# Kernel tuning notes

Hardware: AMD Instinct MI355X
Metric: run time of the kernel (lower is better)

Reference implementation:

```python
import jax, jax.numpy as jnp
import numpy as np

B, N, F, D = 8, 2048, 128, 128


def setup_inputs() -> dict:
    key = jax.random.key(0)
    k1, k2, k3 = jax.random.split(key, 3)
    inputs = jax.random.normal(k1, (B, N, F), dtype=jnp.float32)
    adj = jax.random.uniform(k2, (B, N, N), dtype=jnp.float32)  # nonneg weights -> positive degrees
    W_kernel = jax.random.normal(k3, (F, D), dtype=jnp.float32) * (1.0 / np.sqrt(F))
    W_bias = jnp.zeros((D,), dtype=jnp.float32)
    return {"inputs": inputs, "adj": adj, "W_kernel": W_kernel, "W_bias": W_bias}


def _normalize_adjacency(adj):
    # D^{-1/2} A D^{-1/2}: same math as diag-matmul chain, via broadcast scaling
    d = jnp.sum(adj, axis=-1)                      # [B, N]
    d_sqrt_inv = jnp.power(d, -0.5)
    d_sqrt_inv = jnp.where(jnp.isinf(d_sqrt_inv), 0.0, d_sqrt_inv)
    return d_sqrt_inv[..., :, None] * adj * d_sqrt_inv[..., None, :]


def reference(inputs, adj, W_kernel, W_bias):
    adj_norm = _normalize_adjacency(adj)           # [B, N, N]
    feats = inputs @ W_kernel + W_bias             # [B, N, D]
    out = jnp.einsum('bnm,bmd->bnd', adj_norm, feats)
    return jax.nn.relu(out)
```

## Files before the change

kernel.cpp:

```cpp
#include <hip/hip_runtime.h>
#include <hip/hip_bf16.h>
#include <stdint.h>

#define B_ 8
#define N_ 2048
#define F_ 128
#define D_ 128

typedef short bf16x8 __attribute__((ext_vector_type(8)));
typedef float f32x4 __attribute__((ext_vector_type(4)));

__device__ __forceinline__ unsigned short f2bf(float f) {
    unsigned u = __float_as_uint(f);
    u += 0x7fffu + ((u >> 16) & 1u);
    return (unsigned short)(u >> 16);
}

__global__ __launch_bounds__(256) void k_deg(const float* __restrict__ adj,
                                             float* __restrict__ rs) {
    const int wave = threadIdx.x >> 6, lane = threadIdx.x & 63;
    const int row = blockIdx.x * 4 + wave;
    const float4* p = (const float4*)(adj + (size_t)row * N_);
    float s = 0.f;
#pragma unroll
    for (int j = 0; j < 8; ++j) {
        float4 v = p[j * 64 + lane];
        s += (v.x + v.y) + (v.z + v.w);
    }
#pragma unroll
    for (int m = 1; m < 64; m <<= 1) s += __shfl_xor(s, m, 64);
    if (lane == 0) rs[row] = (s > 0.f) ? (1.0f / sqrtf(s)) : 0.f;
}

__global__ __launch_bounds__(256) void k_feat(const float* __restrict__ x,
                                              const float* __restrict__ W,
                                              const float* __restrict__ bias,
                                              const float* __restrict__ rs,
                                              unsigned short* __restrict__ gt) {
    __shared__ __align__(16) unsigned char sX[64 * 128 * 2];
    __shared__ __align__(16) unsigned char sW[128 * 128 * 2];
    const int t = threadIdx.x;
    const int R0 = blockIdx.x * 64;

#pragma unroll
    for (int j = 0; j < 4; ++j) {
        int c = j * 256 + t;
        int row = c >> 4, sub = c & 15;
        const float4* src = (const float4*)(x + (size_t)(R0 + row) * F_ + sub * 8);
        float4 v0 = src[0], v1 = src[1];
        union { bf16x8 v; unsigned short u[8]; } pk;
        pk.u[0] = f2bf(v0.x); pk.u[1] = f2bf(v0.y); pk.u[2] = f2bf(v0.z); pk.u[3] = f2bf(v0.w);
        pk.u[4] = f2bf(v1.x); pk.u[5] = f2bf(v1.y); pk.u[6] = f2bf(v1.z); pk.u[7] = f2bf(v1.w);
        unsigned byte = (unsigned)(row * 256 + sub * 16);
        byte ^= ((byte >> 8) & 7u) << 4;
        *(bf16x8*)(sX + byte) = pk.v;
    }
#pragma unroll
    for (int j = 0; j < 8; ++j) {
        int c = j * 256 + t;
        int d = c >> 4, sub = c & 15;
        union { bf16x8 v; unsigned short u[8]; } pk;
#pragma unroll
        for (int e = 0; e < 8; ++e) pk.u[e] = f2bf(W[(size_t)(sub * 8 + e) * D_ + d]);
        unsigned byte = (unsigned)(d * 256 + sub * 16);
        byte ^= ((byte >> 8) & 7u) << 4;
        *(bf16x8*)(sW + byte) = pk.v;
    }
    __syncthreads();

    const int w = t >> 6, l = t & 63, lr = l & 15, lh = l >> 4;
    f32x4 acc[8];
#pragma unroll
    for (int j = 0; j < 8; ++j) acc[j] = (f32x4){0.f, 0.f, 0.f, 0.f};

#pragma unroll
    for (int ks = 0; ks < 4; ++ks) {
        int f0 = lh * 8 + ks * 32;
        unsigned abyte = (unsigned)((w * 16 + lr) * 256 + f0 * 2);
        abyte ^= ((abyte >> 8) & 7u) << 4;
        bf16x8 a = *(const bf16x8*)(sX + abyte);
#pragma unroll
        for (int j = 0; j < 8; ++j) {
            unsigned bbyte = (unsigned)((j * 16 + lr) * 256 + f0 * 2);
            bbyte ^= ((bbyte >> 8) & 7u) << 4;
            bf16x8 bb = *(const bf16x8*)(sW + bbyte);
            acc[j] = __builtin_amdgcn_mfma_f32_16x16x32_bf16(a, bb, acc[j], 0, 0, 0);
        }
    }

#pragma unroll
    for (int j = 0; j < 8; ++j) {
        int d = j * 16 + lr;
        float bv = bias[d];
#pragma unroll
        for (int r = 0; r < 4; ++r) {
            int m = R0 + w * 16 + lh * 4 + r;
            float v = (acc[j][r] + bv) * rs[m];
            int b = m >> 11, n = m & (N_ - 1);
            gt[((size_t)b * D_ + d) * N_ + n] = f2bf(v);
        }
    }
}

__global__ __launch_bounds__(256) void k_gcn(const float* __restrict__ adj,
                                             const unsigned short* __restrict__ gt,
                                             const float* __restrict__ rs,
                                             float* __restrict__ out) {
    __shared__ __align__(16) unsigned char sA[2][32 * 64 * 2];
    __shared__ __align__(16) unsigned char sB[2][128 * 64 * 2];

    unsigned bid = blockIdx.x;
    unsigned wg = (bid & 7u) * 64u + (bid >> 3);
    const int b = (int)(wg >> 6);
    const int nt = (int)(wg & 63u);
    const int R0 = nt * 32;

    const float* adjB = adj + (size_t)b * N_ * N_ + (size_t)R0 * N_;
    const unsigned short* gtB = gt + (size_t)b * D_ * N_;

    const int t = threadIdx.x;
    const int w = t >> 6, l = t & 63, lr = l & 15, lh = l >> 4;

    auto stage = [&](int bufidx, int k0) {
        unsigned char* sBb = sB[bufidx];
#pragma unroll
        for (int i = 0; i < 4; ++i) {
            int c = i * 256 + t;
            int d = c >> 3, sub = c & 7;
            int sub2 = sub ^ (d & 7);
            const unsigned short* g = gtB + (size_t)d * N_ + k0 + sub2 * 8;
            __builtin_amdgcn_global_load_lds(
                (const __attribute__((address_space(1))) void*)g,
                (__attribute__((address_space(3))) void*)(sBb + c * 16), 16, 0, 0);
        }
        {
            int c = t;
            int row = c >> 3, sub = c & 7;
            const float4* src = (const float4*)(adjB + (size_t)row * N_ + k0 + sub * 8);
            float4 v0 = src[0], v1 = src[1];
            union { bf16x8 v; unsigned short u[8]; } pk;
            pk.u[0] = f2bf(v0.x); pk.u[1] = f2bf(v0.y); pk.u[2] = f2bf(v0.z); pk.u[3] = f2bf(v0.w);
            pk.u[4] = f2bf(v1.x); pk.u[5] = f2bf(v1.y); pk.u[6] = f2bf(v1.z); pk.u[7] = f2bf(v1.w);
            unsigned byte = (unsigned)(row * 128 + sub * 16);
            byte ^= ((byte >> 7) & 7u) << 4;
            *(bf16x8*)(sA[bufidx] + byte) = pk.v;
        }
    };

    f32x4 acc[2][2];
#pragma unroll
    for (int i = 0; i < 2; ++i)
#pragma unroll
        for (int jn = 0; jn < 2; ++jn) acc[i][jn] = (f32x4){0.f, 0.f, 0.f, 0.f};

    stage(0, 0);
    __syncthreads();

    const int NITER = N_ / 64;
    for (int it = 0; it < NITER; ++it) {
        int cur = it & 1;
        if (it + 1 < NITER) stage(cur ^ 1, (it + 1) * 64);

        const unsigned char* pA = sA[cur];
        const unsigned char* pB = sB[cur];
#pragma unroll
        for (int kk = 0; kk < 2; ++kk) {
            bf16x8 a[2], bb[2];
#pragma unroll
            for (int i = 0; i < 2; ++i) {
                unsigned byte = (unsigned)((i * 16 + lr) * 128 + lh * 16 + kk * 64);
                byte ^= ((byte >> 7) & 7u) << 4;
                a[i] = *(const bf16x8*)(pA + byte);
            }
#pragma unroll
            for (int jn = 0; jn < 2; ++jn) {
                int d = w * 32 + jn * 16 + lr;
                unsigned byte = (unsigned)(d * 128 + lh * 16 + kk * 64);
                byte ^= ((byte >> 7) & 7u) << 4;
                bb[jn] = *(const bf16x8*)(pB + byte);
            }
#pragma unroll
            for (int i = 0; i < 2; ++i)
#pragma unroll
                for (int jn = 0; jn < 2; ++jn)
                    acc[i][jn] = __builtin_amdgcn_mfma_f32_16x16x32_bf16(a[i], bb[jn], acc[i][jn], 0, 0, 0);
        }
        __syncthreads();
    }

#pragma unroll
    for (int i = 0; i < 2; ++i) {
#pragma unroll
        for (int r = 0; r < 4; ++r) {
            int row = i * 16 + lh * 4 + r;
            float rsn = rs[b * N_ + R0 + row];
#pragma unroll
            for (int jn = 0; jn < 2; ++jn) {
                int d = w * 32 + jn * 16 + lr;
                float v = acc[i][jn][r] * rsn;
                out[((size_t)(b * N_ + R0 + row)) * D_ + d] = fmaxf(v, 0.f);
            }
        }
    }
}

extern "C" void kernel_launch(void* const* d_in, const int* in_sizes, int n_in,
                              void* d_out, int out_size, void* d_ws, size_t ws_size,
                              hipStream_t stream) {
    const float* inputs = (const float*)d_in[0];
    const float* adj    = (const float*)d_in[1];
    const float* Wk     = (const float*)d_in[2];
    const float* Wb     = (const float*)d_in[3];
    float* out = (float*)d_out;

    float* rs = (float*)d_ws;
    unsigned short* gt = (unsigned short*)((char*)d_ws + 65536);

    k_deg <<<(B_ * N_) / 4, 256, 0, stream>>>(adj, rs);
    k_feat<<<(B_ * N_) / 64, 256, 0, stream>>>(inputs, Wk, Wb, rs, gt);
    k_gcn <<<B_ * (N_ / 32), 256, 0, stream>>>(adj, gt, rs, out);
}
```

Measured before the change: 67.18 us.

## Pre-transpose W to bf16, move column scaling into adj staging, widen GCN tiles

The degree kernel now also converts W to a transposed bf16 copy once, and k_feat loads it into LDS with direct global-to-LDS loads instead of each block redoing the strided transpose and conversion. The right-side D^{-1/2} scaling moves from the feature GEMM epilogue into the adjacency staging of the GCN kernel, where rs values are multiplied into adj before bf16 conversion. The GCN kernel goes to 512 threads with a 128-wide K step, so each wave owns a 16x32 output tile and there are half as many barriers. This doubles LDS per block and adds a per-element multiply plus extra rs loads in the adj path, which may lower occupancy.

```diff
diff --git a/kernel.cpp b/kernel.cpp
--- a/kernel.cpp
+++ b/kernel.cpp
@@ -16,32 +16,52 @@
     return (unsigned short)(u >> 16);
 }
 
-__global__ __launch_bounds__(256) void k_deg(const float* __restrict__ adj,
-                                             float* __restrict__ rs) {
-    const int wave = threadIdx.x >> 6, lane = threadIdx.x & 63;
-    const int row = blockIdx.x * 4 + wave;
-    const float4* p = (const float4*)(adj + (size_t)row * N_);
-    float s = 0.f;
-#pragma unroll
-    for (int j = 0; j < 8; ++j) {
-        float4 v = p[j * 64 + lane];
-        s += (v.x + v.y) + (v.z + v.w);
-    }
-#pragma unroll
-    for (int m = 1; m < 64; m <<= 1) s += __shfl_xor(s, m, 64);
-    if (lane == 0) rs[row] = (s > 0.f) ? (1.0f / sqrtf(s)) : 0.f;
+__global__ __launch_bounds__(256) void k_degwt(const float* __restrict__ adj,
+                                               const float* __restrict__ W,
+                                               float* __restrict__ rs,
+                                               unsigned short* __restrict__ Wt) {
+    if (blockIdx.x < 4096) {
+        const int wave = threadIdx.x >> 6, lane = threadIdx.x & 63;
+        const int row = blockIdx.x * 4 + wave;
+        const float4* p = (const float4*)(adj + (size_t)row * N_);
+        float s = 0.f;
+#pragma unroll
+        for (int j = 0; j < 8; ++j) {
+            float4 v = p[j * 64 + lane];
+            s += (v.x + v.y) + (v.z + v.w);
+        }
+#pragma unroll
+        for (int m = 1; m < 64; m <<= 1) s += __shfl_xor(s, m, 64);
+        if (lane == 0) rs[row] = (s > 0.f) ? (1.0f / sqrtf(s)) : 0.f;
+    } else {
+        int c = (blockIdx.x - 4096) * 256 + threadIdx.x;
+        int d = c >> 4, f0 = (c & 15) * 8;
+        union { bf16x8 v; unsigned short u[8]; } pk;
+#pragma unroll
+        for (int e = 0; e < 8; ++e) pk.u[e] = f2bf(W[(size_t)(f0 + e) * D_ + d]);
+        *(bf16x8*)(Wt + (size_t)d * F_ + f0) = pk.v;
+    }
 }
 
 __global__ __launch_bounds__(256) void k_feat(const float* __restrict__ x,
-                                              const float* __restrict__ W,
+                                              const unsigned short* __restrict__ Wt,
                                               const float* __restrict__ bias,
-                                              const float* __restrict__ rs,
                                               unsigned short* __restrict__ gt) {
     __shared__ __align__(16) unsigned char sX[64 * 128 * 2];
     __shared__ __align__(16) unsigned char sW[128 * 128 * 2];
     const int t = threadIdx.x;
     const int R0 = blockIdx.x * 64;
 
+#pragma unroll
+    for (int j = 0; j < 8; ++j) {
+        int c = j * 256 + t;
+        unsigned L = (unsigned)c * 16u;
+        unsigned lg = L ^ (((L >> 8) & 7u) << 4);
+        const unsigned char* src = (const unsigned char*)Wt + lg;
+        __builtin_amdgcn_global_load_lds(
+            (const __attribute__((address_space(1))) void*)src,
+            (__attribute__((address_space(3))) void*)(sW + L), 16, 0, 0);
+    }
 #pragma unroll
     for (int j = 0; j < 4; ++j) {
         int c = j * 256 + t;
@@ -55,17 +75,6 @@
         byte ^= ((byte >> 8) & 7u) << 4;
         *(bf16x8*)(sX + byte) = pk.v;
     }
-#pragma unroll
-    for (int j = 0; j < 8; ++j) {
-        int c = j * 256 + t;
-        int d = c >> 4, sub = c & 15;
-        union { bf16x8 v; unsigned short u[8]; } pk;
-#pragma unroll
-        for (int e = 0; e < 8; ++e) pk.u[e] = f2bf(W[(size_t)(sub * 8 + e) * D_ + d]);
-        unsigned byte = (unsigned)(d * 256 + sub * 16);
-        byte ^= ((byte >> 8) & 7u) << 4;
-        *(bf16x8*)(sW + byte) = pk.v;
-    }
     __syncthreads();
 
     const int w = t >> 6, l = t & 63, lr = l & 15, lh = l >> 4;
@@ -95,19 +104,19 @@
 #pragma unroll
         for (int r = 0; r < 4; ++r) {
             int m = R0 + w * 16 + lh * 4 + r;
-            float v = (acc[j][r] + bv) * rs[m];
+            float v = acc[j][r] + bv;
             int b = m >> 11, n = m & (N_ - 1);
             gt[((size_t)b * D_ + d) * N_ + n] = f2bf(v);
         }
     }
 }
 
-__global__ __launch_bounds__(256) void k_gcn(const float* __restrict__ adj,
+__global__ __launch_bounds__(512) void k_gcn(const float* __restrict__ adj,
                                              const unsigned short* __restrict__ gt,
                                              const float* __restrict__ rs,
                                              float* __restrict__ out) {
-    __shared__ __align__(16) unsigned char sA[2][32 * 64 * 2];
-    __shared__ __align__(16) unsigned char sB[2][128 * 64 * 2];
+    __shared__ __align__(16) unsigned char sA[2][32 * 128 * 2];
+    __shared__ __align__(16) unsigned char sB[2][128 * 128 * 2];
 
     unsigned bid = blockIdx.x;
     unsigned wg = (bid & 7u) * 64u + (bid >> 3);
@@ -117,89 +126,83 @@
 
     const float* adjB = adj + (size_t)b * N_ * N_ + (size_t)R0 * N_;
     const unsigned short* gtB = gt + (size_t)b * D_ * N_;
+    const float* rsB = rs + b * N_;
 
     const int t = threadIdx.x;
     const int w = t >> 6, l = t & 63, lr = l & 15, lh = l >> 4;
+    const int wr = (w >> 2) * 16, wc = (w & 3) * 32;
 
     auto stage = [&](int bufidx, int k0) {
         unsigned char* sBb = sB[bufidx];
 #pragma unroll
         for (int i = 0; i < 4; ++i) {
-            int c = i * 256 + t;
-            int d = c >> 3, sub = c & 7;
-            int sub2 = sub ^ (d & 7);
-            const unsigned short* g = gtB + (size_t)d * N_ + k0 + sub2 * 8;
+            int c = i * 512 + t;
+            unsigned L = (unsigned)c * 16u;
+            unsigned lg = L ^ (((L >> 8) & 7u) << 4);
+            int d = (int)(lg >> 8);
+            int mloc = (int)(lg & 255u) >> 1;
+            const unsigned short* g = gtB + (size_t)d * N_ + k0 + mloc;
             __builtin_amdgcn_global_load_lds(
                 (const __attribute__((address_space(1))) void*)g,
-                (__attribute__((address_space(3))) void*)(sBb + c * 16), 16, 0, 0);
+                (__attribute__((address_space(3))) void*)(sBb + L), 16, 0, 0);
         }
         {
-            int c = t;
-            int row = c >> 3, sub = c & 7;
+            int row = t >> 4, sub = t & 15;
             const float4* src = (const float4*)(adjB + (size_t)row * N_ + k0 + sub * 8);
+            const float4* rsm = (const float4*)(rsB + k0 + sub * 8);
             float4 v0 = src[0], v1 = src[1];
+            float4 r0 = rsm[0], r1 = rsm[1];
             union { bf16x8 v; unsigned short u[8]; } pk;
-            pk.u[0] = f2bf(v0.x); pk.u[1] = f2bf(v0.y); pk.u[2] = f2bf(v0.z); pk.u[3] = f2bf(v0.w);
-            pk.u[4] = f2bf(v1.x); pk.u[5] = f2bf(v1.y); pk.u[6] = f2bf(v1.z); pk.u[7] = f2bf(v1.w);
-            unsigned byte = (unsigned)(row * 128 + sub * 16);
-            byte ^= ((byte >> 7) & 7u) << 4;
+            pk.u[0] = f2bf(v0.x * r0.x); pk.u[1] = f2bf(v0.y * r0.y);
+            pk.u[2] = f2bf(v0.z * r0.z); pk.u[3] = f2bf(v0.w * r0.w);
+            pk.u[4] = f2bf(v1.x * r1.x); pk.u[5] = f2bf(v1.y * r1.y);
+            pk.u[6] = f2bf(v1.z * r1.z); pk.u[7] = f2bf(v1.w * r1.w);
+            unsigned byte = (unsigned)(row * 256 + sub * 16);
+            byte ^= ((byte >> 8) & 7u) << 4;
             *(bf16x8*)(sA[bufidx] + byte) = pk.v;
         }
     };
 
-    f32x4 acc[2][2];
-#pragma unroll
-    for (int i = 0; i < 2; ++i)
-#pragma unroll
-        for (int jn = 0; jn < 2; ++jn) acc[i][jn] = (f32x4){0.f, 0.f, 0.f, 0.f};
+    f32x4 acc[2];
+    acc[0] = (f32x4){0.f, 0.f, 0.f, 0.f};
+    acc[1] = (f32x4){0.f, 0.f, 0.f, 0.f};
 
     stage(0, 0);
     __syncthreads();
 
-    const int NITER = N_ / 64;
+    const int NITER = N_ / 128;
     for (int it = 0; it < NITER; ++it) {
         int cur = it & 1;
-        if (it + 1 < NITER) stage(cur ^ 1, (it + 1) * 64);
+        if (it + 1 < NITER) stage(cur ^ 1, (it + 1) * 128);
 
         const unsigned char* pA = sA[cur];
         const unsigned char* pB = sB[cur];
 #pragma unroll
-        for (int kk = 0; kk < 2; ++kk) {
-            bf16x8 a[2], bb[2];
-#pragma unroll
-            for (int i = 0; i < 2; ++i) {
-                unsigned byte = (unsigned)((i * 16 + lr) * 128 + lh * 16 + kk * 64);
-                byte ^= ((byte >> 7) & 7u) << 4;
-                a[i] = *(const bf16x8*)(pA + byte);
+        for (int kk = 0; kk < 4; ++kk) {
+            unsigned abyte = (unsigned)((wr + lr) * 256 + lh * 16 + kk * 64);
+            abyte ^= ((abyte >> 8) & 7u) << 4;
+            bf16x8 a = *(const bf16x8*)(pA + abyte);
+#pragma unroll
+            for (int jn = 0; jn < 2; ++jn) {
+                int d = wc + jn * 16 + lr;
+                unsigned bbyte = (unsigned)(d * 256 + lh * 16 + kk * 64);
+                bbyte ^= ((bbyte >> 8) & 7u) << 4;
+                bf16x8 bb = *(const bf16x8*)(pB + bbyte);
+                acc[jn] = __builtin_amdgcn_mfma_f32_16x16x32_bf16(a, bb, acc[jn], 0, 0, 0);
             }
-#pragma unroll
-            for (int jn = 0; jn < 2; ++jn) {
-                int d = w * 32 + jn * 16 + lr;
-                unsigned byte = (unsigned)(d * 128 + lh * 16 + kk * 64);
-                byte ^= ((byte >> 7) & 7u) << 4;
-                bb[jn] = *(const bf16x8*)(pB + byte);
-            }
-#pragma unroll
-            for (int i = 0; i < 2; ++i)
-#pragma unroll
-                for (int jn = 0; jn < 2; ++jn)
-                    acc[i][jn] = __builtin_amdgcn_mfma_f32_16x16x32_bf16(a[i], bb[jn], acc[i][jn], 0, 0, 0);
         }
         __syncthreads();
     }
 
 #pragma unroll
-    for (int i = 0; i < 2; ++i) {
-#pragma unroll
-        for (int r = 0; r < 4; ++r) {
-            int row = i * 16 + lh * 4 + r;
-            float rsn = rs[b * N_ + R0 + row];
-#pragma unroll
-            for (int jn = 0; jn < 2; ++jn) {
-                int d = w * 32 + jn * 16 + lr;
-                float v = acc[i][jn][r] * rsn;
-                out[((size_t)(b * N_ + R0 + row)) * D_ + d] = fmaxf(v, 0.f);
-            }
+    for (int r = 0; r < 4; ++r) {
+        int row = wr + lh * 4 + r;
+        float rsn = rsB[R0 + row];
+#pragma unroll
+        for (int jn = 0; jn < 2; ++jn) {
+            int d = wc + jn * 16 + lr;
+            float v = acc[jn][r] * rsn;
+            out[((size_t)(b * N_ + R0 + row)) * D_ + d] = fmaxf(v, 0.f);
         }
     }
 }
@@ -215,8 +218,9 @@
 
     float* rs = (float*)d_ws;
     unsigned short* gt = (unsigned short*)((char*)d_ws + 65536);
-
-    k_deg <<<(B_ * N_) / 4, 256, 0, stream>>>(adj, rs);
-    k_feat<<<(B_ * N_) / 64, 256, 0, stream>>>(inputs, Wk, Wb, rs, gt);
-    k_gcn <<<B_ * (N_ / 32), 256, 0, stream>>>(adj, gt, rs, out);
-}
+    unsigned short* Wt = (unsigned short*)((char*)d_ws + 65536 + (size_t)B_ * D_ * N_ * 2);
+
+    k_degwt<<<4096 + 8, 256, 0, stream>>>(adj, Wk, rs, Wt);
+    k_feat <<<(B_ * N_) / 64, 256, 0, stream>>>(inputs, Wt, Wb, gt);
+    k_gcn  <<<B_ * (N_ / 32), 512, 0, stream>>>(adj, gt, rs, out);
+}
```

New measurement: 56.73 us. 1.18x faster.

## Merge degree and feature kernels, restructure GCN matmul with async LDS staging

Applied to the files above, without the earlier changes.

The degree and feature-projection kernels are merged into one launch, and the column D^{-1/2} scaling moves out of the feature kernel into the GCN kernel, which now applies it to fp32 adjacency tiles read from LDS. The GCN kernel switches to 64-row tiles with 512 threads, K-steps of 128, and direct global-to-LDS async loads of fp32 adjacency, with explicit waitcnt/barrier double buffering. The W load is also made coalesced. This aims to cut launch overhead and register-path conversion stalls, at the cost of a large LDS footprint (one block per CU) and only 256 blocks in the main kernel.

```diff
diff --git a/kernel.cpp b/kernel.cpp
--- a/kernel.cpp
+++ b/kernel.cpp
@@ -16,32 +16,48 @@
     return (unsigned short)(u >> 16);
 }
 
-__global__ __launch_bounds__(256) void k_deg(const float* __restrict__ adj,
-                                             float* __restrict__ rs) {
-    const int wave = threadIdx.x >> 6, lane = threadIdx.x & 63;
-    const int row = blockIdx.x * 4 + wave;
-    const float4* p = (const float4*)(adj + (size_t)row * N_);
-    float s = 0.f;
-#pragma unroll
-    for (int j = 0; j < 8; ++j) {
-        float4 v = p[j * 64 + lane];
-        s += (v.x + v.y) + (v.z + v.w);
-    }
-#pragma unroll
-    for (int m = 1; m < 64; m <<= 1) s += __shfl_xor(s, m, 64);
-    if (lane == 0) rs[row] = (s > 0.f) ? (1.0f / sqrtf(s)) : 0.f;
-}
-
-__global__ __launch_bounds__(256) void k_feat(const float* __restrict__ x,
-                                              const float* __restrict__ W,
-                                              const float* __restrict__ bias,
-                                              const float* __restrict__ rs,
-                                              unsigned short* __restrict__ gt) {
+__global__ __launch_bounds__(256) void k_degfeat(const float* __restrict__ adj,
+                                                 const float* __restrict__ x,
+                                                 const float* __restrict__ W,
+                                                 const float* __restrict__ bias,
+                                                 float* __restrict__ rs,
+                                                 unsigned short* __restrict__ gt) {
     __shared__ __align__(16) unsigned char sX[64 * 128 * 2];
     __shared__ __align__(16) unsigned char sW[128 * 128 * 2];
+
     const int t = threadIdx.x;
-    const int R0 = blockIdx.x * 64;
-
+    if (blockIdx.x < 4096) {
+        const int wave = t >> 6, lane = t & 63;
+        const int row = blockIdx.x * 4 + wave;
+        const float4* p = (const float4*)(adj + (size_t)row * N_);
+        float s = 0.f;
+#pragma unroll
+        for (int j = 0; j < 8; ++j) {
+            float4 v = p[j * 64 + lane];
+            s += (v.x + v.y) + (v.z + v.w);
+        }
+#pragma unroll
+        for (int m = 1; m < 64; m <<= 1) s += __shfl_xor(s, m, 64);
+        if (lane == 0) rs[row] = (s > 0.f) ? (1.0f / sqrtf(s)) : 0.f;
+        return;
+    }
+
+    const int R0 = (blockIdx.x - 4096) * 64;
+
+#pragma unroll
+    for (int i = 0; i < 16; ++i) {
+        int c = i * 256 + t;
+        int f = c >> 5, d0 = (c & 31) * 4;
+        float4 v = *(const float4*)(W + (size_t)f * D_ + d0);
+        float vv[4] = {v.x, v.y, v.z, v.w};
+#pragma unroll
+        for (int e = 0; e < 4; ++e) {
+            int dd = d0 + e;
+            unsigned byte = (unsigned)(dd * 256 + f * 2);
+            byte ^= ((byte >> 8) & 15u) << 4;
+            *(unsigned short*)(sW + byte) = f2bf(vv[e]);
+        }
+    }
 #pragma unroll
     for (int j = 0; j < 4; ++j) {
         int c = j * 256 + t;
@@ -55,17 +71,6 @@
         byte ^= ((byte >> 8) & 7u) << 4;
         *(bf16x8*)(sX + byte) = pk.v;
     }
-#pragma unroll
-    for (int j = 0; j < 8; ++j) {
-        int c = j * 256 + t;
-        int d = c >> 4, sub = c & 15;
-        union { bf16x8 v; unsigned short u[8]; } pk;
-#pragma unroll
-        for (int e = 0; e < 8; ++e) pk.u[e] = f2bf(W[(size_t)(sub * 8 + e) * D_ + d]);
-        unsigned byte = (unsigned)(d * 256 + sub * 16);
-        byte ^= ((byte >> 8) & 7u) << 4;
-        *(bf16x8*)(sW + byte) = pk.v;
-    }
     __syncthreads();
 
     const int w = t >> 6, l = t & 63, lr = l & 15, lh = l >> 4;
@@ -75,14 +80,13 @@
 
 #pragma unroll
     for (int ks = 0; ks < 4; ++ks) {
-        int f0 = lh * 8 + ks * 32;
-        unsigned abyte = (unsigned)((w * 16 + lr) * 256 + f0 * 2);
+        unsigned abyte = (unsigned)((w * 16 + lr) * 256 + lh * 16 + ks * 64);
         abyte ^= ((abyte >> 8) & 7u) << 4;
         bf16x8 a = *(const bf16x8*)(sX + abyte);
 #pragma unroll
         for (int j = 0; j < 8; ++j) {
-            unsigned bbyte = (unsigned)((j * 16 + lr) * 256 + f0 * 2);
-            bbyte ^= ((bbyte >> 8) & 7u) << 4;
+            unsigned bbyte = (unsigned)((j * 16 + lr) * 256 + lh * 16 + ks * 64);
+            bbyte ^= ((bbyte >> 8) & 15u) << 4;
             bf16x8 bb = *(const bf16x8*)(sW + bbyte);
             acc[j] = __builtin_amdgcn_mfma_f32_16x16x32_bf16(a, bb, acc[j], 0, 0, 0);
         }
@@ -95,110 +99,142 @@
 #pragma unroll
         for (int r = 0; r < 4; ++r) {
             int m = R0 + w * 16 + lh * 4 + r;
-            float v = (acc[j][r] + bv) * rs[m];
             int b = m >> 11, n = m & (N_ - 1);
-            gt[((size_t)b * D_ + d) * N_ + n] = f2bf(v);
-        }
-    }
-}
-
-__global__ __launch_bounds__(256) void k_gcn(const float* __restrict__ adj,
-                                             const unsigned short* __restrict__ gt,
-                                             const float* __restrict__ rs,
-                                             float* __restrict__ out) {
-    __shared__ __align__(16) unsigned char sA[2][32 * 64 * 2];
-    __shared__ __align__(16) unsigned char sB[2][128 * 64 * 2];
+            gt[((size_t)b * D_ + d) * N_ + n] = f2bf(acc[j][r] + bv);
+        }
+    }
+}
+
+__global__ __launch_bounds__(512, 1) void k_gcn(const float* __restrict__ adj,
+                                                const unsigned short* __restrict__ gt,
+                                                const float* __restrict__ rs,
+                                                float* __restrict__ out) {
+    __shared__ __align__(16) unsigned char sA[2][64 * 128 * 4];
+    __shared__ __align__(16) unsigned char sB[2][128 * 128 * 2];
+    __shared__ __align__(16) unsigned char sRS[N_ * 4];
 
     unsigned bid = blockIdx.x;
-    unsigned wg = (bid & 7u) * 64u + (bid >> 3);
-    const int b = (int)(wg >> 6);
-    const int nt = (int)(wg & 63u);
-    const int R0 = nt * 32;
+    unsigned wg = (bid & 7u) * 32u + (bid >> 3);
+    const int b = (int)(wg >> 5);
+    const int R0 = (int)(wg & 31u) * 64;
 
     const float* adjB = adj + (size_t)b * N_ * N_ + (size_t)R0 * N_;
     const unsigned short* gtB = gt + (size_t)b * D_ * N_;
+    const float* rsB = rs + (size_t)b * N_;
 
     const int t = threadIdx.x;
     const int w = t >> 6, l = t & 63, lr = l & 15, lh = l >> 4;
-
-    auto stage = [&](int bufidx, int k0) {
-        unsigned char* sBb = sB[bufidx];
+    const int wr = w >> 2, wc = w & 3;
+
+    auto stage = [&](int buf, int it) {
+        const int k0 = it * 128;
+        unsigned char* pA = sA[buf];
+        unsigned char* pB = sB[buf];
 #pragma unroll
         for (int i = 0; i < 4; ++i) {
-            int c = i * 256 + t;
-            int d = c >> 3, sub = c & 7;
-            int sub2 = sub ^ (d & 7);
-            const unsigned short* g = gtB + (size_t)d * N_ + k0 + sub2 * 8;
+            unsigned L = (unsigned)(i * 512 + t) * 16u;
+            unsigned row = L >> 9, wi = L & 511u;
+            unsigned wis = wi ^ ((row & 15u) << 4);
+            const unsigned char* g = (const unsigned char*)adjB + (size_t)row * 8192 + (size_t)k0 * 4 + wis;
             __builtin_amdgcn_global_load_lds(
                 (const __attribute__((address_space(1))) void*)g,
-                (__attribute__((address_space(3))) void*)(sBb + c * 16), 16, 0, 0);
-        }
-        {
-            int c = t;
-            int row = c >> 3, sub = c & 7;
-            const float4* src = (const float4*)(adjB + (size_t)row * N_ + k0 + sub * 8);
-            float4 v0 = src[0], v1 = src[1];
-            union { bf16x8 v; unsigned short u[8]; } pk;
-            pk.u[0] = f2bf(v0.x); pk.u[1] = f2bf(v0.y); pk.u[2] = f2bf(v0.z); pk.u[3] = f2bf(v0.w);
-            pk.u[4] = f2bf(v1.x); pk.u[5] = f2bf(v1.y); pk.u[6] = f2bf(v1.z); pk.u[7] = f2bf(v1.w);
-            unsigned byte = (unsigned)(row * 128 + sub * 16);
-            byte ^= ((byte >> 7) & 7u) << 4;
-            *(bf16x8*)(sA[bufidx] + byte) = pk.v;
+                (__attribute__((address_space(3))) void*)(pA + L), 16, 0, 0);
+        }
+#pragma unroll
+        for (int i = 0; i < 4; ++i) {
+            unsigned L = (unsigned)(i * 512 + t) * 16u;
+            unsigned d = L >> 8, wi = L & 255u;
+            unsigned wis = wi ^ ((d & 15u) << 4);
+            const unsigned char* g = (const unsigned char*)gtB + (size_t)d * 4096 + (size_t)k0 * 2 + wis;
+            __builtin_amdgcn_global_load_lds(
+                (const __attribute__((address_space(1))) void*)g,
+                (__attribute__((address_space(3))) void*)(pB + L), 16, 0, 0);
         }
     };
 
+    {
+        unsigned L = (unsigned)t * 16u;
+        __builtin_amdgcn_global_load_lds(
+            (const __attribute__((address_space(1))) void*)((const unsigned char*)rsB + L),
+            (__attribute__((address_space(3))) void*)(sRS + L), 16, 0, 0);
+    }
+    stage(0, 0);
+    stage(1, 1);
+
     f32x4 acc[2][2];
 #pragma unroll
     for (int i = 0; i < 2; ++i)
 #pragma unroll
         for (int jn = 0; jn < 2; ++jn) acc[i][jn] = (f32x4){0.f, 0.f, 0.f, 0.f};
 
-    stage(0, 0);
-    __syncthreads();
-
-    const int NITER = N_ / 64;
+    const int NITER = N_ / 128;
+#pragma unroll
     for (int it = 0; it < NITER; ++it) {
-        int cur = it & 1;
-        if (it + 1 < NITER) stage(cur ^ 1, (it + 1) * 64);
-
-        const unsigned char* pA = sA[cur];
-        const unsigned char* pB = sB[cur];
-#pragma unroll
-        for (int kk = 0; kk < 2; ++kk) {
-            bf16x8 a[2], bb[2];
+        if (it == NITER - 1) {
+            asm volatile("s_waitcnt vmcnt(0)" ::: "memory");
+        } else {
+            asm volatile("s_waitcnt vmcnt(8)" ::: "memory");
+        }
+        __builtin_amdgcn_s_barrier();
+        asm volatile("" ::: "memory");
+        __builtin_amdgcn_sched_barrier(0);
+
+        const unsigned char* pA = sA[it & 1];
+        const unsigned char* pB = sB[it & 1];
+#pragma unroll
+        for (int kk = 0; kk < 4; ++kk) {
+            f32x4 r0 = *(const f32x4*)(sRS + it * 512 + kk * 128 + lh * 32);
+            f32x4 r1 = *(const f32x4*)(sRS + it * 512 + kk * 128 + lh * 32 + 16);
+            bf16x8 av[2];
 #pragma unroll
             for (int i = 0; i < 2; ++i) {
-                unsigned byte = (unsigned)((i * 16 + lr) * 128 + lh * 16 + kk * 64);
-                byte ^= ((byte >> 7) & 7u) << 4;
-                a[i] = *(const bf16x8*)(pA + byte);
+                unsigned row = (unsigned)(wr * 32 + i * 16 + lr);
+                unsigned base = row * 512 + (unsigned)(kk * 128 + lh * 32);
+                unsigned swz = (row & 15u) << 4;
+                f32x4 x0 = *(const f32x4*)(pA + (base ^ swz));
+                f32x4 x1 = *(const f32x4*)(pA + ((base + 16) ^ swz));
+                x0 *= r0; x1 *= r1;
+                unsigned u0, u1, u2, u3;
+                asm("v_cvt_pk_bf16_f32 %0, %1, %2" : "=v"(u0) : "v"(x0[0]), "v"(x0[1]));
+                asm("v_cvt_pk_bf16_f32 %0, %1, %2" : "=v"(u1) : "v"(x0[2]), "v"(x0[3]));
+                asm("v_cvt_pk_bf16_f32 %0, %1, %2" : "=v"(u2) : "v"(x1[0]), "v"(x1[1]));
+                asm("v_cvt_pk_bf16_f32 %0, %1, %2" : "=v"(u3) : "v"(x1[2]), "v"(x1[3]));
+                union { unsigned u[4]; bf16x8 v; } pk;
+                pk.u[0] = u0; pk.u[1] = u1; pk.u[2] = u2; pk.u[3] = u3;
+                av[i] = pk.v;
             }
+            bf16x8 bv[2];
 #pragma unroll
             for (int jn = 0; jn < 2; ++jn) {
-                int d = w * 32 + jn * 16 + lr;
-                unsigned byte = (unsigned)(d * 128 + lh * 16 + kk * 64);
-                byte ^= ((byte >> 7) & 7u) << 4;
-                bb[jn] = *(const bf16x8*)(pB + byte);
+                unsigned d = (unsigned)(wc * 32 + jn * 16 + lr);
+                unsigned byte = d * 256 + (unsigned)(kk * 64 + lh * 16);
+                byte ^= (d & 15u) << 4;
+                bv[jn] = *(const bf16x8*)(pB + byte);
             }
 #pragma unroll
             for (int i = 0; i < 2; ++i)
 #pragma unroll
                 for (int jn = 0; jn < 2; ++jn)
-                    acc[i][jn] = __builtin_amdgcn_mfma_f32_16x16x32_bf16(a[i], bb[jn], acc[i][jn], 0, 0, 0);
-        }
-        __syncthreads();
+                    acc[i][jn] = __builtin_amdgcn_mfma_f32_16x16x32_bf16(av[i], bv[jn], acc[i][jn], 0, 0, 0);
+        }
+
+        asm volatile("s_waitcnt lgkmcnt(0)" ::: "memory");
+        __builtin_amdgcn_sched_barrier(0);
+        __builtin_amdgcn_s_barrier();
+        if (it < NITER - 2) stage(it & 1, it + 2);
     }
 
 #pragma unroll
     for (int i = 0; i < 2; ++i) {
 #pragma unroll
-        for (int r = 0; r < 4; ++r) {
-            int row = i * 16 + lh * 4 + r;
-            float rsn = rs[b * N_ + R0 + row];
+        for (int reg = 0; reg < 4; ++reg) {
+            int rowl = wr * 32 + i * 16 + lh * 4 + reg;
+            float rsn = ((const float*)sRS)[R0 + rowl];
 #pragma unroll
             for (int jn = 0; jn < 2; ++jn) {
-                int d = w * 32 + jn * 16 + lr;
-                float v = acc[i][jn][r] * rsn;
-                out[((size_t)(b * N_ + R0 + row)) * D_ + d] = fmaxf(v, 0.f);
+                int d = wc * 32 + jn * 16 + lr;
+                float v = acc[i][jn][reg] * rsn;
+                out[((size_t)(b * N_ + R0 + rowl)) * D_ + d] = fmaxf(v, 0.f);
             }
         }
     }
@@ -216,7 +252,6 @@
     float* rs = (float*)d_ws;
     unsigned short* gt = (unsigned short*)((char*)d_ws + 65536);
 
-    k_deg <<<(B_ * N_) / 4, 256, 0, stream>>>(adj, rs);
-    k_feat<<<(B_ * N_) / 64, 256, 0, stream>>>(inputs, Wk, Wb, rs, gt);
-    k_gcn <<<B_ * (N_ / 32), 256, 0, stream>>>(adj, gt, rs, out);
-}
+    k_degfeat<<<4096 + 256, 256, 0, stream>>>(adj, inputs, Wk, Wb, rs, gt);
+    k_gcn    <<<256, 512, 0, stream>>>(adj, gt, rs, out);
+}
```

Result: faster. 63.34 us (-5.7%).
